# Kernel optimization log

Hardware: AMD Instinct MI355X
Metric: run time of the kernel (lower is better)

The kernel has to match this reference:

```python
import jax, jax.numpy as jnp
import numpy as np

B, S, DIM = 2, 2048, 2048
H, KVH, HD = 16, 8, 128
NREP = H // KVH


def _make_freqs(seqlen, head_dim):
    # Rotation-matrix form of RoPE: freqs[s,0,p] = [[cos,-sin],[sin,cos]]
    pos = jnp.arange(seqlen, dtype=jnp.float32)
    inv = 1.0 / (10000.0 ** (jnp.arange(0, head_dim, 2, dtype=jnp.float32) / head_dim))
    ang = pos[:, None] * inv[None, :]                      # (S, HD/2)
    cos, sin = jnp.cos(ang), jnp.sin(ang)
    f = jnp.stack([jnp.stack([cos, -sin], -1),
                   jnp.stack([sin, cos], -1)], -2)          # (S, HD/2, 2, 2)
    return f[:, None]                                       # (S, 1, HD/2, 2, 2)


def setup_inputs() -> dict:
    key = jax.random.key(0)
    k0, k1, k2, k3, k4 = jax.random.split(key, 5)
    x = jax.random.normal(k0, (B, S, DIM), jnp.float32)
    x_mask = jnp.ones((B, S), jnp.bool_)                    # unused by forward
    freqs_cis = _make_freqs(S, HD)
    w_qkv = jax.random.normal(k1, ((H + 2 * KVH) * HD, DIM), jnp.float32) * (DIM ** -0.5)
    w_out = jax.random.normal(k2, (DIM, H * HD), jnp.float32) * ((H * HD) ** -0.5)
    q_norm_w = 1.0 + 0.02 * jax.random.normal(k3, (HD,), jnp.float32)
    k_norm_w = 1.0 + 0.02 * jax.random.normal(k4, (HD,), jnp.float32)
    return {"x": x, "x_mask": x_mask, "freqs_cis": freqs_cis,
            "w_qkv": w_qkv, "w_out": w_out,
            "q_norm_w": q_norm_w, "k_norm_w": k_norm_w}


def _rmsnorm(x, w):
    eps = jnp.asarray(jnp.finfo(x.dtype).eps, x.dtype)
    return x * jax.lax.rsqrt(jnp.mean(x * x, -1, keepdims=True) + eps) * w


def _rope(x, freqs):
    # x: (B,S,h,HD), freqs: (S,1,HD/2,2,2)
    t = x.reshape(*x.shape[:-1], HD // 2, 1, 2)
    out = freqs[..., 0] * t[..., 0] + freqs[..., 1] * t[..., 1]
    return out.reshape(x.shape)


def reference(x, x_mask, freqs_cis, w_qkv, w_out, q_norm_w, k_norm_w):
    b, s, _ = x.shape
    qkv = jnp.einsum('bsd,od->bso', x, w_qkv)
    xq, xk, xv = jnp.split(qkv, [H * HD, (H + KVH) * HD], axis=-1)
    xq = _rope(_rmsnorm(xq.reshape(b, s, H, HD), q_norm_w), freqs_cis)
    xk = _rope(_rmsnorm(xk.reshape(b, s, KVH, HD), k_norm_w), freqs_cis)
    xv = xv.reshape(b, s, KVH, HD)
    # GQA: repeat kv heads (consecutive copies, matching unsqueeze+repeat+flatten)
    xk = jnp.repeat(xk, NREP, axis=2)
    xv = jnp.repeat(xv, NREP, axis=2)
    scale = HD ** -0.5
    scores = jnp.einsum('bqhd,bkhd->bhqk', xq, xk) * scale
    attn = jax.nn.softmax(scores, axis=-1)
    out = jnp.einsum('bhqk,bkhd->bqhd', attn, xv).reshape(b, s, H * HD)
    return jnp.einsum('bso,do->bsd', out, w_out)
```

## Files before the change

kernel.cpp:

```cpp
#include <hip/hip_runtime.h>
#include <hip/hip_bf16.h>
#include <cstdint>

typedef __bf16 bf16_t;
typedef __attribute__((ext_vector_type(8)))  __bf16 bf16x8;
typedef __attribute__((ext_vector_type(4)))  float  f32x4;
typedef __attribute__((ext_vector_type(16))) float  f32x16;

#define AS1 __attribute__((address_space(1)))
#define AS3 __attribute__((address_space(3)))
#define DEV __device__ __forceinline__

#define S_BARRIER() asm volatile("s_barrier" ::: "memory")
#define VMCNT0()    asm volatile("s_waitcnt vmcnt(0)" ::: "memory")
#define VMCNT8()    asm volatile("s_waitcnt vmcnt(8)" ::: "memory")
#define SCHED0()    __builtin_amdgcn_sched_barrier(0)

#if __has_builtin(__builtin_amdgcn_exp2f)
#define EXP2(x) __builtin_amdgcn_exp2f(x)
#else
#define EXP2(x) exp2f(x)
#endif

DEV uint32_t pk2bf(float lo, float hi) {
  union { __bf16 h[2]; uint32_t u; } x;
  x.h[0] = (__bf16)lo; x.h[1] = (__bf16)hi; return x.u;
}

__global__ __launch_bounds__(256) void k_cvt3(const float* __restrict__ s0,
                                              const float* __restrict__ s1,
                                              const float* __restrict__ s2,
                                              bf16_t* __restrict__ dst) {
  long i = (long)(blockIdx.x * 256 + threadIdx.x) * 4;
  const float* src;
  long off;
  if (i < 8388608)        { src = s0; off = i; }
  else if (i < 16777216)  { src = s1; off = i - 8388608; }
  else                    { src = s2; off = i - 16777216; }
  const float4 v = *reinterpret_cast<const float4*>(src + off);
  union { bf16_t h[4]; uint2 u; } o;
  o.h[0] = (bf16_t)v.x; o.h[1] = (bf16_t)v.y;
  o.h[2] = (bf16_t)v.z; o.h[3] = (bf16_t)v.w;
  *reinterpret_cast<uint2*>(dst + i) = o.u;
}

#define RD_A_PAIR(dst, base, MF)                                          \
  _Pragma("unroll") for (int j_ = 0; j_ < 2; ++j_)                        \
  _Pragma("unroll") for (int kk_ = 0; kk_ < 2; ++kk_) {                   \
    int p_ = (wm*128 + ((MF)+j_)*16 + c16)*128 + kk_*64 + g*16;           \
    p_ ^= ((p_>>9)&1)<<5;                                                 \
    dst[j_][kk_] = *reinterpret_cast<const bf16x8*>((const char*)(base) + p_); }

#define RD_B_ALL(dst, base)                                               \
  _Pragma("unroll") for (int i_ = 0; i_ < 4; ++i_)                        \
  _Pragma("unroll") for (int kk_ = 0; kk_ < 2; ++kk_) {                   \
    int p_ = (wn*64 + i_*16 + c16)*128 + kk_*64 + g*16;                   \
    p_ ^= ((p_>>9)&1)<<5;                                                 \
    dst[i_][kk_] = *reinterpret_cast<const bf16x8*>((const char*)(base) + p_); }

#define MM_PAIR(aa, MF)                                                   \
  _Pragma("unroll") for (int j_ = 0; j_ < 2; ++j_)                        \
  _Pragma("unroll") for (int i_ = 0; i_ < 4; ++i_)                        \
  _Pragma("unroll") for (int kk_ = 0; kk_ < 2; ++kk_)                     \
    acc[(MF)+j_][i_] = __builtin_amdgcn_mfma_f32_16x16x32_bf16(           \
        aa[j_][kk_], bF[i_][kk_], acc[(MF)+j_][i_], 0, 0, 0);

#define STAGE_A(dstbase, half, tt)                                        \
  _Pragma("unroll") for (int j_ = 0; j_ < 2; ++j_)                        \
    __builtin_amdgcn_global_load_lds(                                     \
        (const AS1 void*)(Ag + srcA[half][j_] + (tt)*64),                 \
        (AS3 void*)((char*)(dstbase) + ((half)*1024 + 512*j_ + wuni)*16), \
        16, 0, 0);

#define STAGE_B(dstbase, half, tt)                                        \
  _Pragma("unroll") for (int j_ = 0; j_ < 2; ++j_)                        \
    __builtin_amdgcn_global_load_lds(                                     \
        (const AS1 void*)(Bg + srcB[half][j_] + (tt)*64),                 \
        (AS3 void*)((char*)(dstbase) + ((half)*1024 + 512*j_ + wuni)*16), \
        16, 0, 0);

__global__ __launch_bounds__(512, 2) void k_gemm256(
    const bf16_t* __restrict__ Ag, const bf16_t* __restrict__ Bg,
    void* __restrict__ Cv, int M, int N, int K, int out_bf16)
{
  extern __shared__ char smemraw[];
  const int tid = threadIdx.x;
  const int w = tid >> 6, l = tid & 63;
  const int wm = w >> 2, wn = w & 3;
  const int c16 = l & 15, g = l >> 4;
  const int wuni = tid & 0x1C0;

  const int nwg = gridDim.x, cpx = nwg >> 3;
  const int bid = blockIdx.x;
  const int L = (bid & 7) * cpx + (bid >> 3);
  const int nbx = N >> 8;
  const int m0 = (L / nbx) * 256, n0 = (L % nbx) * 256;

  int srcA[2][2], srcB[2][2];
#pragma unroll
  for (int half = 0; half < 2; ++half)
#pragma unroll
    for (int j = 0; j < 2; ++j) {
      int ch = half * 1024 + 512 * j + tid;
      int cc = ch ^ (((ch >> 5) & 1) << 1);
      int row = cc >> 3, c8 = (cc & 7) * 8;
      srcA[half][j] = (m0 + row) * K + c8;
      srcB[half][j] = (n0 + row) * K + c8;
    }

  f32x4 acc[8][4] = {};
  bf16x8 aA[2][2], aB[2][2], bF[4][2];

  char* const Ab0 = smemraw;
  char* const Ab1 = smemraw + 32768;
  char* const Bb0 = smemraw + 65536;
  char* const Bb1 = smemraw + 98304;

  const int NT = K >> 6;

  STAGE_A(Ab0, 0, 0); STAGE_A(Ab0, 1, 0);
  STAGE_B(Bb0, 0, 0); STAGE_B(Bb0, 1, 0);
  VMCNT0();
  S_BARRIER();
  RD_A_PAIR(aA, Ab0, 0);
  RD_B_ALL(bF, Bb0);

#pragma unroll 1
  for (int t = 0; t < NT; ++t) {
    char* const Asp = (t & 1) ? Ab1 : Ab0;
    char* const Asn = (t & 1) ? Ab0 : Ab1;
    char* const Bsn = (t & 1) ? Bb0 : Bb1;
    const bool more = (t + 1 < NT);

    RD_A_PAIR(aB, Asp, 2);
    if (more) { STAGE_A(Asn, 0, t + 1); STAGE_A(Asn, 1, t + 1); }
    S_BARRIER();
    __builtin_amdgcn_s_setprio(1);
    MM_PAIR(aA, 0);
    __builtin_amdgcn_s_setprio(0); SCHED0();
    S_BARRIER();

    RD_A_PAIR(aA, Asp, 4);
    if (more) { STAGE_B(Bsn, 0, t + 1); STAGE_B(Bsn, 1, t + 1); }
    S_BARRIER();
    __builtin_amdgcn_s_setprio(1);
    MM_PAIR(aB, 2);
    __builtin_amdgcn_s_setprio(0); SCHED0();
    S_BARRIER();

    RD_A_PAIR(aB, Asp, 6);
    S_BARRIER();
    __builtin_amdgcn_s_setprio(1);
    MM_PAIR(aA, 4);
    __builtin_amdgcn_s_setprio(0); SCHED0();
    S_BARRIER();

    if (more) { VMCNT0(); }
    S_BARRIER();
    __builtin_amdgcn_s_setprio(1);
    MM_PAIR(aB, 6);
    __builtin_amdgcn_s_setprio(0); SCHED0();
    if (more) { RD_A_PAIR(aA, Asn, 0); RD_B_ALL(bF, Bsn); }
    S_BARRIER();
  }

#pragma unroll
  for (int mf = 0; mf < 8; ++mf)
#pragma unroll
    for (int nf = 0; nf < 4; ++nf) {
      const int cc = n0 + wn * 64 + nf * 16 + c16;
#pragma unroll
      for (int r = 0; r < 4; ++r) {
        const int rr = m0 + wm * 128 + mf * 16 + g * 4 + r;
        if (out_bf16)
          ((bf16_t*)Cv)[(size_t)rr * N + cc] = (bf16_t)acc[mf][nf][r];
        else
          ((float*)Cv)[(size_t)rr * N + cc] = acc[mf][nf][r];
      }
    }
}

__global__ __launch_bounds__(256, 2) void k_gemm(
    const bf16_t* __restrict__ A, const bf16_t* __restrict__ B,
    void* __restrict__ Cv, int M, int N, int K, int out_bf16)
{
  __shared__ bf16_t Asl[2][128 * 32];
  __shared__ bf16_t Bsl[2][128 * 32];
  const int tid = threadIdx.x;
  const int w = tid >> 6, l = tid & 63;
  const int wr = w >> 1, wc = w & 1;
  const int c16 = l & 15, g = l >> 4;

  const int nwg = gridDim.x, cpx = nwg >> 3;
  const int bid = blockIdx.x;
  const int L = (bid & 7) * cpx + (bid >> 3);
  const int nbx = N >> 7;
  const int m0 = (L / nbx) * 128, n0 = (L % nbx) * 128;

  const bf16_t* Ab = A + (size_t)m0 * K;
  const bf16_t* Bb = B + (size_t)n0 * K;

  f32x4 acc[4][4] = {};

  auto stage = [&](int buf, int kt) {
    const bf16_t* Ag = Ab + kt * 32;
    const bf16_t* Bg = Bb + kt * 32;
#pragma unroll
    for (int i = 0; i < 2; ++i) {
      int ch = tid + 256 * i;
      int row = ch >> 2, kc = ch & 3;
      __builtin_amdgcn_global_load_lds(
          (const AS1 void*)(Ag + (size_t)row * K + kc * 8),
          (AS3 void*)(&Asl[buf][(w * 64 + 256 * i) * 8]), 16, 0, 0);
      __builtin_amdgcn_global_load_lds(
          (const AS1 void*)(Bg + (size_t)row * K + kc * 8),
          (AS3 void*)(&Bsl[buf][(w * 64 + 256 * i) * 8]), 16, 0, 0);
    }
  };

  auto compute = [&](int buf) {
    bf16x8 af[4], bfg[4];
#pragma unroll
    for (int mi = 0; mi < 4; ++mi)
      af[mi] = *reinterpret_cast<const bf16x8*>(
          &Asl[buf][(wr * 64 + mi * 16 + c16) * 32 + g * 8]);
#pragma unroll
    for (int ni = 0; ni < 4; ++ni)
      bfg[ni] = *reinterpret_cast<const bf16x8*>(
          &Bsl[buf][(wc * 64 + ni * 16 + c16) * 32 + g * 8]);
#pragma unroll
    for (int mi = 0; mi < 4; ++mi)
#pragma unroll
      for (int ni = 0; ni < 4; ++ni)
        acc[mi][ni] = __builtin_amdgcn_mfma_f32_16x16x32_bf16(
            af[mi], bfg[ni], acc[mi][ni], 0, 0, 0);
  };

  const int NT = K >> 5;
  stage(0, 0);
  __syncthreads();
  for (int kt = 0; kt < NT - 1; ++kt) {
    stage((kt + 1) & 1, kt + 1);
    compute(kt & 1);
    __syncthreads();
  }
  compute((NT - 1) & 1);

  const int row0 = m0 + wr * 64, col0 = n0 + wc * 64;
#pragma unroll
  for (int mi = 0; mi < 4; ++mi)
#pragma unroll
    for (int ni = 0; ni < 4; ++ni) {
      const int cc = col0 + ni * 16 + c16;
#pragma unroll
      for (int r = 0; r < 4; ++r) {
        const int rr = row0 + mi * 16 + g * 4 + r;
        if (out_bf16)
          ((bf16_t*)Cv)[(size_t)rr * N + cc] = (bf16_t)acc[mi][ni][r];
        else
          ((float*)Cv)[(size_t)rr * N + cc] = acc[mi][ni][r];
      }
    }
}

__global__ __launch_bounds__(256) void k_prep_qk(
    const bf16_t* __restrict__ qkv, const float* __restrict__ freqs,
    const float* __restrict__ qw, const float* __restrict__ kw,
    bf16_t* __restrict__ Qd, bf16_t* __restrict__ Kd)
{
  const int w = threadIdx.x >> 6, l = threadIdx.x & 63;
  const int R = blockIdx.x * 4 + w;
  const int j = R >> 12;
  const int token = R & 4095;
  const int s = token & 2047, b = token >> 11;
  const bool isq = (j < 16);
  const int col0 = isq ? (j << 7) : (2048 + ((j - 16) << 7));

  union { uint32_t u; __bf16 h[2]; } xin;
  xin.u = *reinterpret_cast<const uint32_t*>(qkv + (size_t)token * 4096 + col0 + 2 * l);
  float x0 = (float)xin.h[0], x1 = (float)xin.h[1];
  float ss = x0 * x0 + x1 * x1;
#pragma unroll
  for (int d = 1; d < 64; d <<= 1) ss += __shfl_xor(ss, d, 64);
  const float rn = rsqrtf(ss * (1.0f / 128.0f) + 1.1920929e-7f);
  const float2 wv = *reinterpret_cast<const float2*>((isq ? qw : kw) + 2 * l);
  const float y0 = x0 * rn * wv.x, y1 = x1 * rn * wv.y;
  const float4 f = *reinterpret_cast<const float4*>(freqs + (size_t)s * 256 + l * 4);
  float o0 = f.x * y0 + f.y * y1;
  float o1 = f.z * y0 + f.w * y1;
  if (isq) { o0 *= 0.1275187989014331f; o1 *= 0.1275187989014331f; }
  const uint32_t pk = pk2bf(o0, o1);
  if (isq)
    *reinterpret_cast<uint32_t*>(Qd + ((size_t)(b * 16 + j) * 2048 + s) * 128 + 2 * l) = pk;
  else
    *reinterpret_cast<uint32_t*>(Kd + ((size_t)(b * 8 + (j - 16)) * 2048 + s) * 128 + 2 * l) = pk;
}

__global__ __launch_bounds__(256) void k_prep_v(const bf16_t* __restrict__ qkv,
                                                bf16_t* __restrict__ Vt)
{
  __shared__ bf16_t vt[64][136];
  const int tid = threadIdx.x;
  const int bid = blockIdx.x;
  const int st = bid & 31, kh = (bid >> 5) & 7, b = bid >> 8;
  const int s0 = st * 64;
#pragma unroll
  for (int i = 0; i < 4; ++i) {
    int ch = tid + 256 * i;
    int srow = ch >> 4, d8 = ch & 15;
    bf16x8 v = *reinterpret_cast<const bf16x8*>(
        qkv + (size_t)(b * 2048 + s0 + srow) * 4096 + 3072 + kh * 128 + d8 * 8);
    *reinterpret_cast<bf16x8*>(&vt[srow][d8 * 8]) = v;
  }
  __syncthreads();
  const int d = tid >> 1, sc = tid & 1;
  bf16_t* dst = Vt + ((size_t)(b * 8 + kh) * 128 + d) * 2048 + s0 + 32 * sc;
#pragma unroll
  for (int grp = 0; grp < 4; ++grp) {
    uint32_t pk[4];
#pragma unroll
    for (int q = 0; q < 4; ++q) {
      int jj = 32 * sc + grp * 8 + q * 2;
      union { __bf16 h[2]; uint32_t u; } e;
      e.h[0] = vt[jj][d]; e.h[1] = vt[jj + 1][d];
      pk[q] = e.u;
    }
    uint4 o; o.x = pk[0]; o.y = pk[1]; o.z = pk[2]; o.w = pk[3];
    *reinterpret_cast<uint4*>(dst + grp * 8) = o;
  }
}

__global__ __launch_bounds__(256, 2) void k_attn(
    const bf16_t* __restrict__ Qd, const bf16_t* __restrict__ Kd,
    const bf16_t* __restrict__ Vt, bf16_t* __restrict__ O)
{
  __shared__ bf16_t kbuf[2][64 * 128];
  __shared__ bf16_t vbuf[2][128 * 64];
  const int tid = threadIdx.x;
  const int w = tid >> 6, l = tid & 63;
  const int c = l & 31, h2 = l >> 5;
  const int bid = blockIdx.x;
  const int qt = bid & 15, h = (bid >> 4) & 15, b = bid >> 8;
  const int kvh = h >> 1;
  const bf16_t* Qg = Qd + ((size_t)(b * 16 + h) * 2048 + qt * 128 + w * 32) * 128;
  const bf16_t* Kg = Kd + ((size_t)(b * 8 + kvh) * 2048) * 128;
  const bf16_t* Vg = Vt + ((size_t)(b * 8 + kvh) * 128) * 2048;

  bf16x8 qf[8];
#pragma unroll
  for (int s = 0; s < 8; ++s)
    qf[s] = *reinterpret_cast<const bf16x8*>(Qg + (size_t)c * 128 + s * 16 + h2 * 8);

  f32x16 oacc[4] = {};
  float l0 = 0.f, l1 = 0.f, l2 = 0.f, l3 = 0.f;

  auto stage = [&](int buf, int kt) {
#pragma unroll
    for (int i = 0; i < 4; ++i) {
      int ch = tid + 256 * i;
      {
        int key = ch >> 4, d16 = ch & 15;
        int soff = key * 256 + ((d16 * 16) ^ ((key & 7) << 4));
        __builtin_amdgcn_global_load_lds(
            (const AS1 void*)((const char*)Kg + (size_t)kt * 64 * 256 + soff),
            (AS3 void*)((char*)&kbuf[buf][0] + (w * 64 + 256 * i) * 16), 16, 0, 0);
      }
      {
        int d = ch >> 3, k8 = (ch & 7) ^ (d & 7);
        __builtin_amdgcn_global_load_lds(
            (const AS1 void*)(Vg + (size_t)d * 2048 + kt * 64 + k8 * 8),
            (AS3 void*)((char*)&vbuf[buf][0] + (w * 64 + 256 * i) * 16), 16, 0, 0);
      }
    }
  };

  auto compute = [&](int buf) {
    f32x16 sacc[2] = {};
    const char* kb = (const char*)&kbuf[buf][0];
    __builtin_amdgcn_s_setprio(1);
#pragma unroll
    for (int m = 0; m < 2; ++m)
#pragma unroll
      for (int s = 0; s < 8; ++s) {
        int byte = (m * 32 + c) * 256 + ((s * 32 + h2 * 16) ^ ((c & 7) << 4));
        bf16x8 kf = *reinterpret_cast<const bf16x8*>(kb + byte);
        sacc[m] = __builtin_amdgcn_mfma_f32_32x32x16_bf16(kf, qf[s], sacc[m], 0, 0, 0);
      }
    __builtin_amdgcn_s_setprio(0);

#pragma unroll
    for (int m = 0; m < 2; ++m)
#pragma unroll
      for (int r = 0; r < 16; r += 4) {
        float p0 = EXP2(sacc[m][r + 0]);
        float p1 = EXP2(sacc[m][r + 1]);
        float p2 = EXP2(sacc[m][r + 2]);
        float p3 = EXP2(sacc[m][r + 3]);
        sacc[m][r + 0] = p0; sacc[m][r + 1] = p1;
        sacc[m][r + 2] = p2; sacc[m][r + 3] = p3;
        l0 += p0; l1 += p1; l2 += p2; l3 += p3;
      }

    const char* vb = (const char*)&vbuf[buf][0];
#pragma unroll
    for (int t = 0; t < 4; ++t) {
      const int m = t >> 1, q2i = t & 1;
      uint32_t u0 = pk2bf(sacc[m][8 * q2i + 0], sacc[m][8 * q2i + 1]);
      uint32_t u1 = pk2bf(sacc[m][8 * q2i + 2], sacc[m][8 * q2i + 3]);
      uint32_t u2 = pk2bf(sacc[m][8 * q2i + 4], sacc[m][8 * q2i + 5]);
      uint32_t u3 = pk2bf(sacc[m][8 * q2i + 6], sacc[m][8 * q2i + 7]);
      auto r02 = __builtin_amdgcn_permlane32_swap((int)u0, (int)u2, false, false);
      auto r13 = __builtin_amdgcn_permlane32_swap((int)u1, (int)u3, false, false);
      union { uint32_t u[4]; bf16x8 v; } pb;
      pb.u[0] = (uint32_t)r02[0]; pb.u[1] = (uint32_t)r13[0];
      pb.u[2] = (uint32_t)r02[1]; pb.u[3] = (uint32_t)r13[1];
      __builtin_amdgcn_s_setprio(1);
#pragma unroll
      for (int df = 0; df < 4; ++df) {
        int byte = (df * 32 + c) * 128 + ((t * 32 + h2 * 16) ^ ((c & 7) << 4));
        bf16x8 vf = *reinterpret_cast<const bf16x8*>(vb + byte);
        oacc[df] = __builtin_amdgcn_mfma_f32_32x32x16_bf16(vf, pb.v, oacc[df], 0, 0, 0);
      }
      __builtin_amdgcn_s_setprio(0);
    }
  };

  stage(0, 0);
#pragma unroll 1
  for (int kt = 0; kt < 31; ++kt) {
    stage((kt + 1) & 1, kt + 1);
    VMCNT8();
    S_BARRIER();
    compute(kt & 1);
    S_BARRIER();
  }
  VMCNT0();
  S_BARRIER();
  compute(1);

  float lrun = (l0 + l1) + (l2 + l3);
  lrun += __shfl_xor(lrun, 32, 64);
  const float inv = 1.0f / lrun;
  bf16_t* Og = O + ((size_t)(b * 2048 + qt * 128 + w * 32 + c) * 2048) + h * 128;
#pragma unroll
  for (int df = 0; df < 4; ++df)
#pragma unroll
    for (int rg = 0; rg < 4; ++rg) {
      uint32_t w0 = pk2bf(oacc[df][rg * 4 + 0] * inv, oacc[df][rg * 4 + 1] * inv);
      uint32_t w1 = pk2bf(oacc[df][rg * 4 + 2] * inv, oacc[df][rg * 4 + 3] * inv);
      uint2 ww; ww.x = w0; ww.y = w1;
      *reinterpret_cast<uint2*>(Og + df * 32 + 8 * rg + 4 * h2) = ww;
    }
}

extern "C" void kernel_launch(void* const* d_in, const int* in_sizes, int n_in,
                              void* d_out, int out_size, void* d_ws, size_t ws_size,
                              hipStream_t stream)
{
  const float* x     = (const float*)d_in[0];
  const float* freqs = (const float*)d_in[2];
  const float* wqkv  = (const float*)d_in[3];
  const float* wout  = (const float*)d_in[4];
  const float* qw    = (const float*)d_in[5];
  const float* kw    = (const float*)d_in[6];
  float* out = (float*)d_out;

  bf16_t* Xb   = (bf16_t*)d_ws;
  bf16_t* Wqb  = Xb  + 8388608;
  bf16_t* Wob  = Wqb + 8388608;
  bf16_t* qkvb = Wob + 4194304;
  bf16_t* Qdp  = qkvb + 16777216;
  bf16_t* Kdp  = Qdp + 8388608;
  bf16_t* Vtp  = Kdp + 4194304;
  bf16_t* Ob   = qkvb;

  (void)hipFuncSetAttribute((const void*)k_gemm256,
                            hipFuncAttributeMaxDynamicSharedMemorySize, 131072);

  k_cvt3<<<20480, 256, 0, stream>>>(x, wqkv, wout, Xb);
  k_gemm256<<<256, 512, 131072, stream>>>(Xb, Wqb, qkvb, 4096, 4096, 2048, 1);
  k_prep_qk<<<24576, 256, 0, stream>>>(qkvb, freqs, qw, kw, Qdp, Kdp);
  k_prep_v<<<512, 256, 0, stream>>>(qkvb, Vtp);
  k_attn<<<512, 256, 0, stream>>>(Qdp, Kdp, Vtp, Ob);
  k_gemm<<<512, 256, 0, stream>>>(Ob, Wob, out, 4096, 2048, 2048, 0);
}
```

Baseline: 237.9 us.

## Replace output-projection GEMM with 256x128 pipelined tile kernel and merge prep kernels

Replaces the simple 128x128, K=32 double-buffered output-projection GEMM with a 512-thread kernel that computes 256x128 tiles. It uses K=64 stages loaded straight into swizzled LDS, interleaves LDS reads with MFMA phases and raises wave priority around the MFMA blocks, modelled on the existing QKV GEMM. The aim is more data reuse per tile and better overlap of memory loads with matrix math. It also fuses the Q/K norm+RoPE prep and the V transpose into one launch to save a kernel launch, at the cost of a larger shared-memory footprint that lowers occupancy and a branch inside the merged prep kernel.

```diff
diff --git a/kernel.cpp b/kernel.cpp
--- a/kernel.cpp
+++ b/kernel.cpp
@@ -58,6 +58,13 @@
     p_ ^= ((p_>>9)&1)<<5;                                                 \
     dst[i_][kk_] = *reinterpret_cast<const bf16x8*>((const char*)(base) + p_); }
 
+#define RD_B2(dst, base)                                                  \
+  _Pragma("unroll") for (int i_ = 0; i_ < 2; ++i_)                        \
+  _Pragma("unroll") for (int kk_ = 0; kk_ < 2; ++kk_) {                   \
+    int p_ = (wn*32 + i_*16 + c16)*128 + kk_*64 + g*16;                   \
+    p_ ^= ((p_>>9)&1)<<5;                                                 \
+    dst[i_][kk_] = *reinterpret_cast<const bf16x8*>((const char*)(base) + p_); }
+
 #define MM_PAIR(aa, MF)                                                   \
   _Pragma("unroll") for (int j_ = 0; j_ < 2; ++j_)                        \
   _Pragma("unroll") for (int i_ = 0; i_ < 4; ++i_)                        \
@@ -65,6 +72,13 @@
     acc[(MF)+j_][i_] = __builtin_amdgcn_mfma_f32_16x16x32_bf16(           \
         aa[j_][kk_], bF[i_][kk_], acc[(MF)+j_][i_], 0, 0, 0);
 
+#define MM_PAIR2(aa, MF)                                                  \
+  _Pragma("unroll") for (int j_ = 0; j_ < 2; ++j_)                        \
+  _Pragma("unroll") for (int i_ = 0; i_ < 2; ++i_)                        \
+  _Pragma("unroll") for (int kk_ = 0; kk_ < 2; ++kk_)                     \
+    acc[(MF)+j_][i_] = __builtin_amdgcn_mfma_f32_16x16x32_bf16(           \
+        aa[j_][kk_], bG[i_][kk_], acc[(MF)+j_][i_], 0, 0, 0);
+
 #define STAGE_A(dstbase, half, tt)                                        \
   _Pragma("unroll") for (int j_ = 0; j_ < 2; ++j_)                        \
     __builtin_amdgcn_global_load_lds(                                     \
@@ -78,6 +92,12 @@
         (const AS1 void*)(Bg + srcB[half][j_] + (tt)*64),                 \
         (AS3 void*)((char*)(dstbase) + ((half)*1024 + 512*j_ + wuni)*16), \
         16, 0, 0);
+
+#define STAGE_B2(dstbase, tt)                                             \
+  _Pragma("unroll") for (int j_ = 0; j_ < 2; ++j_)                        \
+    __builtin_amdgcn_global_load_lds(                                     \
+        (const AS1 void*)(Bg + srcB2[j_] + (tt)*64),                      \
+        (AS3 void*)((char*)(dstbase) + (512*j_ + wuni)*16), 16, 0, 0);
 
 __global__ __launch_bounds__(512, 2) void k_gemm256(
     const bf16_t* __restrict__ Ag, const bf16_t* __restrict__ Bg,
@@ -180,153 +200,174 @@
     }
 }
 
-__global__ __launch_bounds__(256, 2) void k_gemm(
-    const bf16_t* __restrict__ A, const bf16_t* __restrict__ B,
-    void* __restrict__ Cv, int M, int N, int K, int out_bf16)
+__global__ __launch_bounds__(512, 2) void k_og(
+    const bf16_t* __restrict__ Ag, const bf16_t* __restrict__ Bg,
+    float* __restrict__ Cv, int M, int N, int K)
 {
-  __shared__ bf16_t Asl[2][128 * 32];
-  __shared__ bf16_t Bsl[2][128 * 32];
+  extern __shared__ char smemraw[];
   const int tid = threadIdx.x;
   const int w = tid >> 6, l = tid & 63;
-  const int wr = w >> 1, wc = w & 1;
+  const int wm = w >> 2, wn = w & 3;
   const int c16 = l & 15, g = l >> 4;
+  const int wuni = tid & 0x1C0;
 
   const int nwg = gridDim.x, cpx = nwg >> 3;
   const int bid = blockIdx.x;
   const int L = (bid & 7) * cpx + (bid >> 3);
   const int nbx = N >> 7;
-  const int m0 = (L / nbx) * 128, n0 = (L % nbx) * 128;
-
-  const bf16_t* Ab = A + (size_t)m0 * K;
-  const bf16_t* Bb = B + (size_t)n0 * K;
-
-  f32x4 acc[4][4] = {};
-
-  auto stage = [&](int buf, int kt) {
-    const bf16_t* Ag = Ab + kt * 32;
-    const bf16_t* Bg = Bb + kt * 32;
-#pragma unroll
-    for (int i = 0; i < 2; ++i) {
-      int ch = tid + 256 * i;
-      int row = ch >> 2, kc = ch & 3;
-      __builtin_amdgcn_global_load_lds(
-          (const AS1 void*)(Ag + (size_t)row * K + kc * 8),
-          (AS3 void*)(&Asl[buf][(w * 64 + 256 * i) * 8]), 16, 0, 0);
-      __builtin_amdgcn_global_load_lds(
-          (const AS1 void*)(Bg + (size_t)row * K + kc * 8),
-          (AS3 void*)(&Bsl[buf][(w * 64 + 256 * i) * 8]), 16, 0, 0);
-    }
-  };
-
-  auto compute = [&](int buf) {
-    bf16x8 af[4], bfg[4];
-#pragma unroll
-    for (int mi = 0; mi < 4; ++mi)
-      af[mi] = *reinterpret_cast<const bf16x8*>(
-          &Asl[buf][(wr * 64 + mi * 16 + c16) * 32 + g * 8]);
-#pragma unroll
-    for (int ni = 0; ni < 4; ++ni)
-      bfg[ni] = *reinterpret_cast<const bf16x8*>(
-          &Bsl[buf][(wc * 64 + ni * 16 + c16) * 32 + g * 8]);
-#pragma unroll
-    for (int mi = 0; mi < 4; ++mi)
-#pragma unroll
-      for (int ni = 0; ni < 4; ++ni)
-        acc[mi][ni] = __builtin_amdgcn_mfma_f32_16x16x32_bf16(
-            af[mi], bfg[ni], acc[mi][ni], 0, 0, 0);
-  };
-
-  const int NT = K >> 5;
-  stage(0, 0);
-  __syncthreads();
-  for (int kt = 0; kt < NT - 1; ++kt) {
-    stage((kt + 1) & 1, kt + 1);
-    compute(kt & 1);
-    __syncthreads();
+  const int m0 = (L / nbx) * 256, n0 = (L % nbx) * 128;
+
+  int srcA[2][2], srcB2[2];
+#pragma unroll
+  for (int half = 0; half < 2; ++half)
+#pragma unroll
+    for (int j = 0; j < 2; ++j) {
+      int ch = half * 1024 + 512 * j + tid;
+      int cc = ch ^ (((ch >> 5) & 1) << 1);
+      int row = cc >> 3, c8 = (cc & 7) * 8;
+      srcA[half][j] = (m0 + row) * K + c8;
+    }
+#pragma unroll
+  for (int j = 0; j < 2; ++j) {
+    int ch = 512 * j + tid;
+    int cc = ch ^ (((ch >> 5) & 1) << 1);
+    int row = cc >> 3, c8 = (cc & 7) * 8;
+    srcB2[j] = (n0 + row) * K + c8;
   }
-  compute((NT - 1) & 1);
-
-  const int row0 = m0 + wr * 64, col0 = n0 + wc * 64;
-#pragma unroll
-  for (int mi = 0; mi < 4; ++mi)
-#pragma unroll
-    for (int ni = 0; ni < 4; ++ni) {
-      const int cc = col0 + ni * 16 + c16;
+
+  f32x4 acc[8][2] = {};
+  bf16x8 aA[2][2], aB[2][2], bG[2][2];
+
+  char* const Ab0 = smemraw;
+  char* const Ab1 = smemraw + 32768;
+  char* const Bb0 = smemraw + 65536;
+  char* const Bb1 = smemraw + 81920;
+
+  const int NT = K >> 6;
+
+  STAGE_A(Ab0, 0, 0); STAGE_A(Ab0, 1, 0);
+  STAGE_B2(Bb0, 0);
+  VMCNT0();
+  S_BARRIER();
+  RD_A_PAIR(aA, Ab0, 0);
+  RD_B2(bG, Bb0);
+
+#pragma unroll 1
+  for (int t = 0; t < NT; ++t) {
+    char* const Asp = (t & 1) ? Ab1 : Ab0;
+    char* const Asn = (t & 1) ? Ab0 : Ab1;
+    char* const Bsn = (t & 1) ? Bb0 : Bb1;
+    const bool more = (t + 1 < NT);
+
+    RD_A_PAIR(aB, Asp, 2);
+    if (more) { STAGE_A(Asn, 0, t + 1); STAGE_A(Asn, 1, t + 1); }
+    S_BARRIER();
+    __builtin_amdgcn_s_setprio(1);
+    MM_PAIR2(aA, 0);
+    __builtin_amdgcn_s_setprio(0); SCHED0();
+    S_BARRIER();
+
+    RD_A_PAIR(aA, Asp, 4);
+    if (more) { STAGE_B2(Bsn, t + 1); }
+    S_BARRIER();
+    __builtin_amdgcn_s_setprio(1);
+    MM_PAIR2(aB, 2);
+    __builtin_amdgcn_s_setprio(0); SCHED0();
+    S_BARRIER();
+
+    RD_A_PAIR(aB, Asp, 6);
+    S_BARRIER();
+    __builtin_amdgcn_s_setprio(1);
+    MM_PAIR2(aA, 4);
+    __builtin_amdgcn_s_setprio(0); SCHED0();
+    S_BARRIER();
+
+    if (more) { VMCNT0(); }
+    S_BARRIER();
+    __builtin_amdgcn_s_setprio(1);
+    MM_PAIR2(aB, 6);
+    __builtin_amdgcn_s_setprio(0); SCHED0();
+    if (more) { RD_A_PAIR(aA, Asn, 0); RD_B2(bG, Bsn); }
+    S_BARRIER();
+  }
+
+#pragma unroll
+  for (int mf = 0; mf < 8; ++mf)
+#pragma unroll
+    for (int nf = 0; nf < 2; ++nf) {
+      const int cc = n0 + wn * 32 + nf * 16 + c16;
 #pragma unroll
       for (int r = 0; r < 4; ++r) {
-        const int rr = row0 + mi * 16 + g * 4 + r;
-        if (out_bf16)
-          ((bf16_t*)Cv)[(size_t)rr * N + cc] = (bf16_t)acc[mi][ni][r];
-        else
-          ((float*)Cv)[(size_t)rr * N + cc] = acc[mi][ni][r];
-      }
-    }
-}
-
-__global__ __launch_bounds__(256) void k_prep_qk(
+        const int rr = m0 + wm * 128 + mf * 16 + g * 4 + r;
+        Cv[(size_t)rr * N + cc] = acc[mf][nf][r];
+      }
+    }
+}
+
+__global__ __launch_bounds__(256) void k_prep(
     const bf16_t* __restrict__ qkv, const float* __restrict__ freqs,
     const float* __restrict__ qw, const float* __restrict__ kw,
-    bf16_t* __restrict__ Qd, bf16_t* __restrict__ Kd)
-{
-  const int w = threadIdx.x >> 6, l = threadIdx.x & 63;
-  const int R = blockIdx.x * 4 + w;
-  const int j = R >> 12;
-  const int token = R & 4095;
-  const int s = token & 2047, b = token >> 11;
-  const bool isq = (j < 16);
-  const int col0 = isq ? (j << 7) : (2048 + ((j - 16) << 7));
-
-  union { uint32_t u; __bf16 h[2]; } xin;
-  xin.u = *reinterpret_cast<const uint32_t*>(qkv + (size_t)token * 4096 + col0 + 2 * l);
-  float x0 = (float)xin.h[0], x1 = (float)xin.h[1];
-  float ss = x0 * x0 + x1 * x1;
-#pragma unroll
-  for (int d = 1; d < 64; d <<= 1) ss += __shfl_xor(ss, d, 64);
-  const float rn = rsqrtf(ss * (1.0f / 128.0f) + 1.1920929e-7f);
-  const float2 wv = *reinterpret_cast<const float2*>((isq ? qw : kw) + 2 * l);
-  const float y0 = x0 * rn * wv.x, y1 = x1 * rn * wv.y;
-  const float4 f = *reinterpret_cast<const float4*>(freqs + (size_t)s * 256 + l * 4);
-  float o0 = f.x * y0 + f.y * y1;
-  float o1 = f.z * y0 + f.w * y1;
-  if (isq) { o0 *= 0.1275187989014331f; o1 *= 0.1275187989014331f; }
-  const uint32_t pk = pk2bf(o0, o1);
-  if (isq)
-    *reinterpret_cast<uint32_t*>(Qd + ((size_t)(b * 16 + j) * 2048 + s) * 128 + 2 * l) = pk;
-  else
-    *reinterpret_cast<uint32_t*>(Kd + ((size_t)(b * 8 + (j - 16)) * 2048 + s) * 128 + 2 * l) = pk;
-}
-
-__global__ __launch_bounds__(256) void k_prep_v(const bf16_t* __restrict__ qkv,
-                                                bf16_t* __restrict__ Vt)
+    bf16_t* __restrict__ Qd, bf16_t* __restrict__ Kd,
+    bf16_t* __restrict__ Vt)
 {
   __shared__ bf16_t vt[64][136];
-  const int tid = threadIdx.x;
   const int bid = blockIdx.x;
-  const int st = bid & 31, kh = (bid >> 5) & 7, b = bid >> 8;
-  const int s0 = st * 64;
-#pragma unroll
-  for (int i = 0; i < 4; ++i) {
-    int ch = tid + 256 * i;
-    int srow = ch >> 4, d8 = ch & 15;
-    bf16x8 v = *reinterpret_cast<const bf16x8*>(
-        qkv + (size_t)(b * 2048 + s0 + srow) * 4096 + 3072 + kh * 128 + d8 * 8);
-    *reinterpret_cast<bf16x8*>(&vt[srow][d8 * 8]) = v;
-  }
-  __syncthreads();
-  const int d = tid >> 1, sc = tid & 1;
-  bf16_t* dst = Vt + ((size_t)(b * 8 + kh) * 128 + d) * 2048 + s0 + 32 * sc;
-#pragma unroll
-  for (int grp = 0; grp < 4; ++grp) {
-    uint32_t pk[4];
-#pragma unroll
-    for (int q = 0; q < 4; ++q) {
-      int jj = 32 * sc + grp * 8 + q * 2;
-      union { __bf16 h[2]; uint32_t u; } e;
-      e.h[0] = vt[jj][d]; e.h[1] = vt[jj + 1][d];
-      pk[q] = e.u;
-    }
-    uint4 o; o.x = pk[0]; o.y = pk[1]; o.z = pk[2]; o.w = pk[3];
-    *reinterpret_cast<uint4*>(dst + grp * 8) = o;
+  if (bid < 24576) {
+    const int w = threadIdx.x >> 6, l = threadIdx.x & 63;
+    const int R = bid * 4 + w;
+    const int j = R >> 12;
+    const int token = R & 4095;
+    const int s = token & 2047, b = token >> 11;
+    const bool isq = (j < 16);
+    const int col0 = isq ? (j << 7) : (2048 + ((j - 16) << 7));
+
+    union { uint32_t u; __bf16 h[2]; } xin;
+    xin.u = *reinterpret_cast<const uint32_t*>(qkv + (size_t)token * 4096 + col0 + 2 * l);
+    float x0 = (float)xin.h[0], x1 = (float)xin.h[1];
+    float ss = x0 * x0 + x1 * x1;
+#pragma unroll
+    for (int d = 1; d < 64; d <<= 1) ss += __shfl_xor(ss, d, 64);
+    const float rn = rsqrtf(ss * (1.0f / 128.0f) + 1.1920929e-7f);
+    const float2 wv = *reinterpret_cast<const float2*>((isq ? qw : kw) + 2 * l);
+    const float y0 = x0 * rn * wv.x, y1 = x1 * rn * wv.y;
+    const float4 f = *reinterpret_cast<const float4*>(freqs + (size_t)s * 256 + l * 4);
+    float o0 = f.x * y0 + f.y * y1;
+    float o1 = f.z * y0 + f.w * y1;
+    if (isq) { o0 *= 0.1275187989014331f; o1 *= 0.1275187989014331f; }
+    const uint32_t pk = pk2bf(o0, o1);
+    if (isq)
+      *reinterpret_cast<uint32_t*>(Qd + ((size_t)(b * 16 + j) * 2048 + s) * 128 + 2 * l) = pk;
+    else
+      *reinterpret_cast<uint32_t*>(Kd + ((size_t)(b * 8 + (j - 16)) * 2048 + s) * 128 + 2 * l) = pk;
+  } else {
+    const int vb = bid - 24576;
+    const int tid = threadIdx.x;
+    const int st = vb & 31, kh = (vb >> 5) & 7, b = vb >> 8;
+    const int s0 = st * 64;
+#pragma unroll
+    for (int i = 0; i < 4; ++i) {
+      int ch = tid + 256 * i;
+      int srow = ch >> 4, d8 = ch & 15;
+      bf16x8 v = *reinterpret_cast<const bf16x8*>(
+          qkv + (size_t)(b * 2048 + s0 + srow) * 4096 + 3072 + kh * 128 + d8 * 8);
+      *reinterpret_cast<bf16x8*>(&vt[srow][d8 * 8]) = v;
+    }
+    __syncthreads();
+    const int d = tid >> 1, sc = tid & 1;
+    bf16_t* dst = Vt + ((size_t)(b * 8 + kh) * 128 + d) * 2048 + s0 + 32 * sc;
+#pragma unroll
+    for (int grp = 0; grp < 4; ++grp) {
+      uint32_t pk[4];
+#pragma unroll
+      for (int q = 0; q < 4; ++q) {
+        int jj = 32 * sc + grp * 8 + q * 2;
+        union { __bf16 h[2]; uint32_t u; } e;
+        e.h[0] = vt[jj][d]; e.h[1] = vt[jj + 1][d];
+        pk[q] = e.u;
+      }
+      uint4 o; o.x = pk[0]; o.y = pk[1]; o.z = pk[2]; o.w = pk[3];
+      *reinterpret_cast<uint4*>(dst + grp * 8) = o;
+    }
   }
 }
 
@@ -476,11 +517,12 @@
 
   (void)hipFuncSetAttribute((const void*)k_gemm256,
                             hipFuncAttributeMaxDynamicSharedMemorySize, 131072);
+  (void)hipFuncSetAttribute((const void*)k_og,
+                            hipFuncAttributeMaxDynamicSharedMemorySize, 98304);
 
   k_cvt3<<<20480, 256, 0, stream>>>(x, wqkv, wout, Xb);
   k_gemm256<<<256, 512, 131072, stream>>>(Xb, Wqb, qkvb, 4096, 4096, 2048, 1);
-  k_prep_qk<<<24576, 256, 0, stream>>>(qkvb, freqs, qw, kw, Qdp, Kdp);
-  k_prep_v<<<512, 256, 0, stream>>>(qkvb, Vtp);
+  k_prep<<<25088, 256, 0, stream>>>(qkvb, freqs, qw, kw, Qdp, Kdp, Vtp);
   k_attn<<<512, 256, 0, stream>>>(Qdp, Kdp, Vtp, Ob);
-  k_gemm<<<512, 256, 0, stream>>>(Ob, Wob, out, 4096, 2048, 2048, 0);
-}
+  k_og<<<256, 512, 98304, stream>>>(Ob, Wob, out, 4096, 2048, 2048);
+}
```

Result: faster. 230.0 us (-3.3%).
